# Kernel optimization log

Hardware: AMD Instinct MI355X
Metric: run time of the kernel (lower is better)

The kernel has to match this reference:

```python
import jax, jax.numpy as jnp
import numpy as np

B, W, CBLK, C, H, L, VOCAB = 8, 512, 24, 512, 8, 2, 256
HD = C // H


def _ln(x, g, b, eps=1e-5):
    m = x.mean(-1, keepdims=True)
    v = ((x - m) ** 2).mean(-1, keepdims=True)
    return (x - m) * jax.lax.rsqrt(v + eps) * g + b


def _causal_attn(q, k, v):
    # q,k,v: [..., T, hd]; causal softmax attention, scale 1/sqrt(hd)
    T = q.shape[-2]
    scale = 1.0 / (q.shape[-1] ** 0.5)
    s = jnp.einsum('...qd,...kd->...qk', q, k) * scale
    mask = jnp.tril(jnp.ones((T, T), dtype=bool))
    s = jnp.where(mask, s, jnp.finfo(s.dtype).min)
    return jnp.einsum('...qk,...kd->...qd', jax.nn.softmax(s, axis=-1), v)


def _mha_char(seq, w_qkv, last_ix):
    # seq: [B,W,c,C]; per-word causal char attention, then gather row last_ix
    b, w, c, _ = seq.shape
    q, k, v = jnp.split(seq @ w_qkv, 3, axis=-1)
    sh = lambda t: t.reshape(b, w, c, H, HD).transpose(0, 1, 3, 2, 4)
    o = _causal_attn(sh(q), sh(k), sh(v))          # [B,W,H,c,hd]
    o = o.transpose(0, 1, 3, 2, 4).reshape(b, w, c, C)
    return jnp.take_along_axis(o, last_ix[:, :, None, None], axis=2)[:, :, 0, :]


def _mha_word(x, w_qkv, w_proj):
    b, w, _ = x.shape
    q, k, v = jnp.split(x @ w_qkv, 3, axis=-1)
    sh = lambda t: t.reshape(b, w, H, HD).transpose(0, 2, 1, 3)
    o = _causal_attn(sh(q), sh(k), sh(v))
    o = o.transpose(0, 2, 1, 3).reshape(b, w, C)
    return o @ w_proj


def setup_inputs() -> dict:
    key = jax.random.key(0)
    ks = jax.random.split(key, 16)
    # ragged word lengths in [1, CBLK]; mask = ones then zeros (as produced by pad())
    lengths = jax.random.randint(ks[0], (B, W), 1, CBLK + 1)
    attention_mask = (jnp.arange(CBLK)[None, None, :] < lengths[:, :, None]).astype(jnp.int32)
    x = jax.random.randint(ks[1], (B, W, CBLK), 0, VOCAB).astype(jnp.int32)
    std = 0.02
    res_std = std * (2 * L) ** -0.5  # res_flag init scaling
    n = lambda k, s, sd=std: sd * jax.random.normal(k, s, dtype=jnp.float32)
    return dict(
        x=x, attention_mask=attention_mask,
        cte=n(ks[2], (VOCAB, C)), cpe=n(ks[3], (CBLK, C)), wpe=n(ks[4], (W, C)),
        ln1_g=jnp.ones((L, C)), ln1_b=jnp.zeros((L, C)),
        ln2_g=jnp.ones((L, C)), ln2_b=jnp.zeros((L, C)),
        ln3_g=jnp.ones((L, C)), ln3_b=jnp.zeros((L, C)),
        cattn_w=n(ks[5], (L, C, 3 * C)), cattn_proj=n(ks[6], (L, C, C)),
        wattn_w=n(ks[7], (L, C, 3 * C)), wattn_proj=n(ks[8], (L, C, C), res_std),
        mlp_fc=n(ks[9], (L, C, 4 * C)), mlp_proj=n(ks[10], (L, 4 * C, C), res_std),
        proj_w=n(ks[11], (C, CBLK * C)), lm_head_w=n(ks[12], (C, VOCAB)),
    )


def reference(x, attention_mask, cte, cpe, wpe, ln1_g, ln1_b, ln2_g, ln2_b, ln3_g, ln3_b,
              cattn_w, cattn_proj, wattn_w, wattn_proj, mlp_fc, mlp_proj, proj_w, lm_head_w):
    last_ix = attention_mask.sum(axis=2) - 1           # [B,W], last real char per word
    state = cte[x] + cpe[None, None, :, :]             # [B,W,c,C]
    context = None                                     # current_conv.context/pad, vectorized
    for l in range(L):
        if l == 0:
            # first_time: operate on full padded char sequences, cache ln_1 output
            hln = _ln(state, ln1_g[l], ln1_b[l])       # [B,W,c,C]
            context = hln
            seq = hln
        else:
            # splice the new word vector into position last_ix of the cached context
            hln = _ln(state, ln1_g[l], ln1_b[l])       # [B,W,C]
            repl = jnp.arange(CBLK)[None, None, :] == last_ix[:, :, None]
            seq = jnp.where(repl[..., None], hln[:, :, None, :], context)
        o = _mha_char(seq, cattn_w[l], last_ix)        # [B,W,C]
        if l == 0:
            o = o + wpe[None, :, :]                    # word pos emb added only first_time
        state = o @ cattn_proj[l]                      # note: no residual around c_attn
        state = state + _mha_word(_ln(state, ln2_g[l], ln2_b[l]), wattn_w[l], wattn_proj[l])
        hm = _ln(state, ln3_g[l], ln3_b[l])
        state = state + jax.nn.gelu(hm @ mlp_fc[l], approximate=False) @ mlp_proj[l]
    y = (state @ proj_w).reshape(B, W, CBLK, C)
    return y @ lm_head_w                               # logits [B,W,CBLK,VOCAB]
```

## Files before the change

kernel.cpp:

```cpp
#include <hip/hip_runtime.h>
#include <hip/hip_bf16.h>
#include <math.h>


namespace {

constexpr int Bn = 8, Wn = 512, CB = 24, Cd = 512, Hn = 8, Lln = 2, Vn = 256, HDn = 64;
constexpr int BW = Bn * Wn;
constexpr int C3 = 3 * Cd;
constexpr int FF = 4 * Cd;
constexpr int NROW = BW * CB;

typedef unsigned short u16;
typedef short short8 __attribute__((ext_vector_type(8)));
typedef float f32x4 __attribute__((ext_vector_type(4)));
typedef __attribute__((address_space(1))) void gvoid_t;
typedef __attribute__((address_space(3))) void lvoid_t;

__device__ __forceinline__ u16 f2bu(float f) {
  __hip_bfloat16 h = __float2bfloat16(f);
  return __builtin_bit_cast(u16, h);
}
__device__ __forceinline__ float bu2f(u16 u) {
  return __bfloat162float(__builtin_bit_cast(__hip_bfloat16, u));
}
__device__ __forceinline__ float geluf(float x) {
  return 0.5f * x * (1.0f + erff(x * 0.7071067811865475f));
}
__device__ __forceinline__ void gl16(const void* g, void* l) {
  __builtin_amdgcn_global_load_lds((gvoid_t*)g, (lvoid_t*)l, 16, 0, 0);
}

__global__ void k_lastix(const int* __restrict__ mask, int* __restrict__ lastix) {
  int i = blockIdx.x * 256 + threadIdx.x;
  if (i < BW) {
    int s = 0;
#pragma unroll
    for (int j = 0; j < CB; ++j) s += mask[i * CB + j];
    lastix[i] = s - 1;
  }
}

__device__ __forceinline__ void f2b8(const float* __restrict__ s, u16* __restrict__ d) {
  float4 a = *(const float4*)s;
  float4 b = *(const float4*)(s + 4);
  union { uint4 u; u16 h[8]; } pk;
  pk.h[0] = f2bu(a.x); pk.h[1] = f2bu(a.y); pk.h[2] = f2bu(a.z); pk.h[3] = f2bu(a.w);
  pk.h[4] = f2bu(b.x); pk.h[5] = f2bu(b.y); pk.h[6] = f2bu(b.z); pk.h[7] = f2bu(b.w);
  *(uint4*)d = pk.u;
}

__device__ __forceinline__ void wT_tile(const float* __restrict__ src, u16* __restrict__ dst,
                                        int K, int N, int n0, int k0,
                                        u16 T[64][72], int tid) {
  int kl = tid >> 2, nc = (tid & 3) * 16;
  const float* s = src + (long)(k0 + kl) * N + n0 + nc;
#pragma unroll
  for (int u = 0; u < 4; ++u) {
    float4 f = *(const float4*)(s + u * 4);
    T[nc + u * 4 + 0][kl] = f2bu(f.x);
    T[nc + u * 4 + 1][kl] = f2bu(f.y);
    T[nc + u * 4 + 2][kl] = f2bu(f.z);
    T[nc + u * 4 + 3][kl] = f2bu(f.w);
  }
  __syncthreads();
  int nl = tid >> 2, kc = (tid & 3) * 16;
  u16* d = dst + (long)(n0 + nl) * K + k0 + kc;
  *(uint4*)d = *(uint4*)&T[nl][kc];
  *(uint4*)(d + 8) = *(uint4*)&T[nl][kc + 8];
}

__global__ __launch_bounds__(256) void k_prep(
    const float* __restrict__ proj_w, u16* __restrict__ projwb,
    const float* __restrict__ cattn_w, u16* __restrict__ wcb,
    const float* __restrict__ lm_head, u16* __restrict__ lmhT,
    const float* __restrict__ cattn_proj, const float* __restrict__ wattn_w,
    const float* __restrict__ wattn_proj, const float* __restrict__ mlp_fc,
    const float* __restrict__ mlp_proj, u16* __restrict__ wT) {
  __shared__ u16 T[64][72];
  int b = blockIdx.x, tid = threadIdx.x;
  if (b < 3072) { long i = ((long)b * 256 + tid) * 8; f2b8(proj_w + i, projwb + i); return; }
  b -= 3072;
  if (b < 768) { long i = ((long)b * 256 + tid) * 8; f2b8(cattn_w + i, wcb + i); return; }
  b -= 768;
  if (b < 32) { wT_tile(lm_head, lmhT, Cd, Vn, (b & 3) * 64, (b >> 2) * 64, T, tid); return; }
  b -= 32;
  int l = b >> 10, r = b & 1023;
  size_t lw = (size_t)(2 * C3 * Cd + 2 * Cd * Cd + 2 * FF * Cd);
  u16* bl = wT + l * lw;
  const float* src; u16* dst; int K, N, nt;
  if (r < 192)      { src = cattn_w + (size_t)l * Cd * C3;    dst = bl;                              K = Cd; N = C3; nt = 24; }
  else if (r < 256) { src = cattn_proj + (size_t)l * Cd * Cd; dst = bl + C3 * Cd;                    K = Cd; N = Cd; nt = 8;  r -= 192; }
  else if (r < 448) { src = wattn_w + (size_t)l * Cd * C3;    dst = bl + C3 * Cd + Cd * Cd;          K = Cd; N = C3; nt = 24; r -= 256; }
  else if (r < 512) { src = wattn_proj + (size_t)l * Cd * Cd; dst = bl + 2 * C3 * Cd + Cd * Cd;      K = Cd; N = Cd; nt = 8;  r -= 448; }
  else if (r < 768) { src = mlp_fc + (size_t)l * Cd * FF;     dst = bl + 2 * C3 * Cd + 2 * Cd * Cd;  K = Cd; N = FF; nt = 32; r -= 512; }
  else              { src = mlp_proj + (size_t)l * FF * Cd;   dst = bl + 2 * C3 * Cd + 2 * Cd * Cd + FF * Cd; K = FF; N = Cd; nt = 8; r -= 768; }
  wT_tile(src, dst, K, N, (r % nt) * 64, (r / nt) * 64, T, tid);
}

__global__ __launch_bounds__(64) void k_embed_ln(
    const int* __restrict__ x, const float* __restrict__ cte, const float* __restrict__ cpe,
    const float* __restrict__ g, const float* __restrict__ b,
    const int* __restrict__ lastix, u16* __restrict__ ctx) {
  int r = blockIdx.x;
  int bw = r / CB, ch = r - bw * CB;
  if (ch > lastix[bw]) return;
  int tok = x[r];
  const float* e = cte + (long)tok * Cd;
  const float* pe = cpe + (long)ch * Cd;
  int lane = threadIdx.x;
  float v[8];
  float s = 0.f, sq = 0.f;
#pragma unroll
  for (int u = 0; u < 2; ++u) {
    float4 a = *(const float4*)(e + u * 256 + lane * 4);
    float4 p4 = *(const float4*)(pe + u * 256 + lane * 4);
    v[u * 4 + 0] = a.x + p4.x; v[u * 4 + 1] = a.y + p4.y;
    v[u * 4 + 2] = a.z + p4.z; v[u * 4 + 3] = a.w + p4.w;
  }
#pragma unroll
  for (int u = 0; u < 8; ++u) { s += v[u]; sq += v[u] * v[u]; }
#pragma unroll
  for (int m = 32; m; m >>= 1) { s += __shfl_xor(s, m); sq += __shfl_xor(sq, m); }
  float mean = s * (1.0f / Cd);
  float var = sq * (1.0f / Cd) - mean * mean;
  float rs = rsqrtf(var + 1e-5f);
  u16* o = ctx + (long)r * Cd;
#pragma unroll
  for (int u = 0; u < 2; ++u) {
    int c0 = u * 256 + lane * 4;
    float4 g4 = *(const float4*)(g + c0);
    float4 b4 = *(const float4*)(b + c0);
    float o0 = (v[u * 4 + 0] - mean) * rs * g4.x + b4.x;
    float o1 = (v[u * 4 + 1] - mean) * rs * g4.y + b4.y;
    float o2 = (v[u * 4 + 2] - mean) * rs * g4.z + b4.z;
    float o3 = (v[u * 4 + 3] - mean) * rs * g4.w + b4.w;
    uint2 w;
    w.x = (unsigned)f2bu(o0) | ((unsigned)f2bu(o1) << 16);
    w.y = (unsigned)f2bu(o2) | ((unsigned)f2bu(o3) << 16);
    *(uint2*)(o + c0) = w;
  }
}

__global__ __launch_bounds__(64) void k_ln(
    const float* __restrict__ X, u16* __restrict__ Y,
    const float* __restrict__ g, const float* __restrict__ b) {
  long r = blockIdx.x;
  const float* xr = X + r * Cd;
  int lane = threadIdx.x;
  float v[8];
  float s = 0.f, sq = 0.f;
#pragma unroll
  for (int u = 0; u < 2; ++u) {
    float4 a = *(const float4*)(xr + u * 256 + lane * 4);
    v[u * 4 + 0] = a.x; v[u * 4 + 1] = a.y; v[u * 4 + 2] = a.z; v[u * 4 + 3] = a.w;
  }
#pragma unroll
  for (int u = 0; u < 8; ++u) { s += v[u]; sq += v[u] * v[u]; }
#pragma unroll
  for (int m = 32; m; m >>= 1) { s += __shfl_xor(s, m); sq += __shfl_xor(sq, m); }
  float mean = s * (1.0f / Cd);
  float var = sq * (1.0f / Cd) - mean * mean;
  float rs = rsqrtf(var + 1e-5f);
  u16* o = Y + r * Cd;
#pragma unroll
  for (int u = 0; u < 2; ++u) {
    int c0 = u * 256 + lane * 4;
    float4 g4 = *(const float4*)(g + c0);
    float4 b4 = *(const float4*)(b + c0);
    float o0 = (v[u * 4 + 0] - mean) * rs * g4.x + b4.x;
    float o1 = (v[u * 4 + 1] - mean) * rs * g4.y + b4.y;
    float o2 = (v[u * 4 + 2] - mean) * rs * g4.z + b4.z;
    float o3 = (v[u * 4 + 3] - mean) * rs * g4.w + b4.w;
    uint2 w;
    w.x = (unsigned)f2bu(o0) | ((unsigned)f2bu(o1) << 16);
    w.y = (unsigned)f2bu(o2) | ((unsigned)f2bu(o3) << 16);
    *(uint2*)(o + c0) = w;
  }
}

__global__ __launch_bounds__(64) void k_gather_last(
    const u16* __restrict__ ctx, const int* __restrict__ lastix, u16* __restrict__ qin) {
  long bw = blockIdx.x;
  int r = (int)bw * CB + lastix[bw];
  const uint4* s = (const uint4*)(ctx + (long)r * Cd);
  uint4* d = (uint4*)(qin + bw * Cd);
  d[threadIdx.x] = s[threadIdx.x];
}

template <int BM, int BN, int EPI, int OUTBF>
__global__ __launch_bounds__(256) void k_mgemm(
    const u16* __restrict__ A, int lda, long sA1, long sA2,
    const u16* __restrict__ Bt, int ldb, long sB1, long sB2,
    void* __restrict__ Cv, int ldc, long sC1, long sC2,
    const float* __restrict__ R, u16* __restrict__ D2,
    const float* __restrict__ PL, const u16* __restrict__ VL,
    const float* __restrict__ WP, int K, int zdiv) {
  constexpr int WM = BM / 2;
  constexpr int WN = BN / 2;
  constexpr int FM = WM / 16, FN = WN / 16;
  __shared__ u16 As[BM * 32];
  __shared__ u16 Bs[BN * 32];
  long m0 = (long)blockIdx.y * BM, n0 = (long)blockIdx.x * BN;
  int z = blockIdx.z;
  int z1 = z / zdiv, z2 = z - z1 * zdiv;
  A += z1 * sA1 + z2 * sA2;
  Bt += z1 * sB1 + z2 * sB2;
  long coff = z1 * sC1 + z2 * sC2;
  int tid = threadIdx.x;
  int wid = tid >> 6, lane = tid & 63;
  int wr = wid >> 1, wc = wid & 1;

  const int srow = tid >> 2, skk = (tid & 3) * 8;
  const u16* Ald[BM / 64];
  const u16* Bld[BN / 64];
#pragma unroll
  for (int i = 0; i < BM / 64; ++i) Ald[i] = A + (m0 + srow + i * 64) * (long)lda + skk;
#pragma unroll
  for (int i = 0; i < BN / 64; ++i) Bld[i] = Bt + (n0 + srow + i * 64) * (long)ldb + skk;

  f32x4 acc[FM][FN] = {};
  const int fr = lane & 15, kg = lane >> 4;

  for (int k0 = 0; k0 < K; k0 += 32) {
#pragma unroll
    for (int i = 0; i < BM / 64; ++i) gl16(Ald[i] + k0, &As[(tid + i * 256) * 8]);
#pragma unroll
    for (int i = 0; i < BN / 64; ++i) gl16(Bld[i] + k0, &Bs[(tid + i * 256) * 8]);
    __syncthreads();
    short8 af[FM], bf[FN];
#pragma unroll
    for (int m = 0; m < FM; ++m)
      af[m] = *(const short8*)&As[(wr * WM + m * 16 + fr) * 32 + kg * 8];
#pragma unroll
    for (int n = 0; n < FN; ++n)
      bf[n] = *(const short8*)&Bs[(wc * WN + n * 16 + fr) * 32 + kg * 8];
#pragma unroll
    for (int m = 0; m < FM; ++m)
#pragma unroll
      for (int n = 0; n < FN; ++n)
        acc[m][n] = __builtin_amdgcn_mfma_f32_16x16x32_bf16(af[m], bf[n], acc[m][n], 0, 0, 0);
    __syncthreads();
  }
  int ccol = lane & 15, crow4 = (lane >> 4) * 4;
#pragma unroll
  for (int m = 0; m < FM; ++m)
#pragma unroll
    for (int n = 0; n < FN; ++n)
#pragma unroll
      for (int q = 0; q < 4; ++q) {
        long gr = m0 + wr * WM + m * 16 + crow4 + q;
        long gc = n0 + wc * WN + n * 16 + ccol;
        float v = acc[m][n][q];
        long idx = gr * (long)ldc + gc + coff;
        if (EPI == 1 || EPI == 3) v += R[idx];
        if (EPI == 2) v = geluf(v);
        if (EPI == 4) {
          v += PL[gr * 8 + z2] * bu2f(VL[gr * (long)C3 + 2 * Cd + z2 * 64 + gc]);
          if (WP) v += WP[(long)(gr & (Wn - 1)) * Cd + z2 * 64 + gc];
        }
        if (EPI == 3) {
          ((float*)Cv)[idx] = v;
          D2[idx] = f2bu(v);
        } else if (OUTBF) {
          ((u16*)Cv)[idx] = f2bu(v);
        } else {
          ((float*)Cv)[idx] = v;
        }
      }
}

__global__ __launch_bounds__(256) void k_cattn2(
    const u16* __restrict__ ctx, const u16* __restrict__ qtil,
    const u16* __restrict__ qkvc, const int* __restrict__ lastix,
    u16* __restrict__ U, float* __restrict__ plast) {
  constexpr int CS = 520;
  int gw = blockIdx.x;
  int li = lastix[gw];
  __shared__ u16 ctxs[CB - 1][CS];
  __shared__ float spf[4][Hn][32];
  __shared__ float sp[Hn][CB];
  int tid = threadIdx.x;
  for (int u = tid; u < li * 64; u += 256) {
    int row = u >> 6, c = (u & 63) * 8;
    *(uint4*)&ctxs[row][c] = *(const uint4*)(ctx + ((long)(gw * CB + row)) * Cd + c);
  }
  __syncthreads();
  int w = tid >> 6, lane = tid & 63;
  int fr = lane & 15, kg = lane >> 4;
  {
    const u16* qbase = qtil + (long)gw * 4096 + (fr & 7) * 512 + w * 128 + kg * 8;
    int r0 = fr;
    int r1 = 16 + fr; if (r1 > CB - 2) r1 = CB - 2;
    f32x4 acc0 = {}, acc1 = {};
#pragma unroll
    for (int kk = 0; kk < 4; ++kk) {
      short8 af = *(const short8*)(qbase + kk * 32);
      short8 b0 = *(const short8*)&ctxs[r0][w * 128 + kk * 32 + kg * 8];
      short8 b1 = *(const short8*)&ctxs[r1][w * 128 + kk * 32 + kg * 8];
      acc0 = __builtin_amdgcn_mfma_f32_16x16x32_bf16(af, b0, acc0, 0, 0, 0);
      acc1 = __builtin_amdgcn_mfma_f32_16x16x32_bf16(af, b1, acc1, 0, 0, 0);
    }
    if (lane < 32) {
      int jj = lane & 15;
#pragma unroll
      for (int q = 0; q < 4; ++q) {
        int h = (lane >> 4) * 4 + q;
        spf[w][h][jj] = acc0[q];
        spf[w][h][16 + jj] = acc1[q];
      }
    }
  }
  __syncthreads();
  {
    int h = tid >> 5, j = tid & 31;
    if (j < CB)
      sp[h][j] = (spf[0][h][j] + spf[1][h][j] + spf[2][h][j] + spf[3][h][j]) * 0.125f;
  }
  __syncthreads();
  if (tid < 8) {
    const u16* qq = qkvc + (long)gw * C3 + tid * 64;
    const u16* kk = qq + Cd;
    float s = 0.f;
#pragma unroll
    for (int u = 0; u < 64; ++u) s += bu2f(qq[u]) * bu2f(kk[u]);
    sp[tid][li] = s * 0.125f;
  }
  __syncthreads();
  if (tid < 8) {
    float m = -3.4e38f;
    for (int jj = 0; jj <= li; ++jj) m = fmaxf(m, sp[tid][jj]);
    float s = 0.f;
    for (int jj = 0; jj <= li; ++jj) { float e = expf(sp[tid][jj] - m); sp[tid][jj] = e; s += e; }
    float inv = 1.0f / s;
    for (int jj = 0; jj <= li; ++jj) sp[tid][jj] *= inv;
    plast[gw * 8 + tid] = sp[tid][li];
  }
  __syncthreads();
  int h = tid >> 5, d0 = (tid & 31) * 16;
  float uacc[16];
#pragma unroll
  for (int i = 0; i < 16; ++i) uacc[i] = 0.f;
  for (int jj = 0; jj < li; ++jj) {
    float p = sp[h][jj];
    const u16* cv = &ctxs[jj][d0];
#pragma unroll
    for (int i = 0; i < 16; ++i) uacc[i] += p * bu2f(cv[i]);
  }
  union { uint4 q[2]; u16 hh[16]; } pk;
#pragma unroll
  for (int i = 0; i < 16; ++i) pk.hh[i] = f2bu(uacc[i]);
  u16* d = U + (long)gw * 4096 + h * 512 + d0;
  *(uint4*)d = pk.q[0];
  *(uint4*)(d + 8) = pk.q[1];
}

__global__ __launch_bounds__(256) void k_vt(const u16* __restrict__ qkv, u16* __restrict__ Vt) {
  __shared__ u16 T[64][72];
  int z = blockIdx.y, jt = blockIdx.x;
  int b = z >> 3, h = z & 7;
  int tid = threadIdx.x;
  int jl = tid >> 2, dc = (tid & 3) * 16;
  const u16* s = qkv + ((long)(b * Wn + jt * 64 + jl)) * C3 + 2 * Cd + h * HDn + dc;
  *(uint4*)&T[jl][dc] = *(const uint4*)s;
  *(uint4*)&T[jl][dc + 8] = *(const uint4*)(s + 8);
  __syncthreads();
  int dl = tid >> 2, jc = (tid & 3) * 16;
  u16 tmp[16];
#pragma unroll
  for (int u = 0; u < 16; ++u) tmp[u] = T[jc + u][dl];
  u16* d = Vt + (long)z * HDn * Wn + (long)dl * Wn + jt * 64 + jc;
  *(uint4*)d = *(uint4*)&tmp[0];
  *(uint4*)(d + 8) = *(uint4*)&tmp[8];
}

__global__ __launch_bounds__(256) void k_fattn(
    const u16* __restrict__ qkv, const u16* __restrict__ Vt, u16* __restrict__ ao) {
  constexpr int ST = 68;
  __shared__ u16 Ks[64 * ST];
  __shared__ u16 Vs[64 * ST];
  __shared__ u16 Ps[4][16 * ST];
  int qt = blockIdx.x;
  int z  = blockIdx.y;
  int b = z >> 3, h = z & 7;
  int tid = threadIdx.x;
  int w = tid >> 6, lane = tid & 63;
  int fr = lane & 15, kg = lane >> 4;

  short8 qf[2];
  {
    const u16* qp = qkv + ((long)(b * Wn + qt * 64 + w * 16 + fr)) * C3 + h * 64 + kg * 8;
    qf[0] = *(const short8*)qp;
    qf[1] = *(const short8*)(qp + 32);
  }
  f32x4 oacc[4] = {};
  float mrow[4], lrow[4];
#pragma unroll
  for (int q = 0; q < 4; ++q) { mrow[q] = -3.4e38f; lrow[q] = 0.f; }

  for (int kt = 0; kt <= qt; ++kt) {
    __syncthreads();
    {
      int r = tid >> 2, c = (tid & 3) * 16;
      const u16* kp = qkv + ((long)(b * Wn + kt * 64 + r)) * C3 + Cd + h * 64 + c;
      *(uint4*)&Ks[r * ST + c] = *(const uint4*)kp;
      *(uint4*)&Ks[r * ST + c + 8] = *(const uint4*)(kp + 8);
      const u16* vp = Vt + (long)z * (64 * Wn) + (long)r * Wn + kt * 64 + c;
      *(uint4*)&Vs[r * ST + c] = *(const uint4*)vp;
      *(uint4*)&Vs[r * ST + c + 8] = *(const uint4*)(vp + 8);
    }
    __syncthreads();
    f32x4 s[4];
#pragma unroll
    for (int n = 0; n < 4; ++n) {
      short8 kf0 = *(const short8*)&Ks[(n * 16 + fr) * ST + kg * 8];
      short8 kf1 = *(const short8*)&Ks[(n * 16 + fr) * ST + kg * 8 + 32];
      f32x4 a = {};
      a = __builtin_amdgcn_mfma_f32_16x16x32_bf16(qf[0], kf0, a, 0, 0, 0);
      a = __builtin_amdgcn_mfma_f32_16x16x32_bf16(qf[1], kf1, a, 0, 0, 0);
      s[n] = a;
    }
    int irow0 = qt * 64 + w * 16 + kg * 4;
#pragma unroll
    for (int n = 0; n < 4; ++n) {
      int jcol = kt * 64 + n * 16 + fr;
#pragma unroll
      for (int q = 0; q < 4; ++q) {
        float v = s[n][q] * 0.125f;
        s[n][q] = (jcol > irow0 + q) ? -3.4e38f : v;
      }
    }
    float sf[4];
#pragma unroll
    for (int q = 0; q < 4; ++q) {
      float mm = fmaxf(fmaxf(s[0][q], s[1][q]), fmaxf(s[2][q], s[3][q]));
      mm = fmaxf(mm, __shfl_xor(mm, 1));
      mm = fmaxf(mm, __shfl_xor(mm, 2));
      mm = fmaxf(mm, __shfl_xor(mm, 4));
      mm = fmaxf(mm, __shfl_xor(mm, 8));
      float mnew = fmaxf(mrow[q], mm);
      sf[q] = expf(mrow[q] - mnew);
      mrow[q] = mnew;
    }
    float ls[4] = {0.f, 0.f, 0.f, 0.f};
#pragma unroll
    for (int n = 0; n < 4; ++n) {
#pragma unroll
      for (int q = 0; q < 4; ++q) {
        float p = expf(s[n][q] - mrow[q]);
        u16 pb = f2bu(p);
        ls[q] += bu2f(pb);
        Ps[w][(kg * 4 + q) * ST + n * 16 + fr] = pb;
      }
    }
#pragma unroll
    for (int q = 0; q < 4; ++q) {
      float l = ls[q];
      l += __shfl_xor(l, 1); l += __shfl_xor(l, 2);
      l += __shfl_xor(l, 4); l += __shfl_xor(l, 8);
      lrow[q] = lrow[q] * sf[q] + l;
#pragma unroll
      for (int n = 0; n < 4; ++n) oacc[n][q] *= sf[q];
    }
    asm volatile("s_waitcnt lgkmcnt(0)" ::: "memory");
    short8 pa0 = *(const short8*)&Ps[w][fr * ST + kg * 8];
    short8 pa1 = *(const short8*)&Ps[w][fr * ST + kg * 8 + 32];
#pragma unroll
    for (int n = 0; n < 4; ++n) {
      short8 vf0 = *(const short8*)&Vs[(n * 16 + fr) * ST + kg * 8];
      short8 vf1 = *(const short8*)&Vs[(n * 16 + fr) * ST + kg * 8 + 32];
      oacc[n] = __builtin_amdgcn_mfma_f32_16x16x32_bf16(pa0, vf0, oacc[n], 0, 0, 0);
      oacc[n] = __builtin_amdgcn_mfma_f32_16x16x32_bf16(pa1, vf1, oacc[n], 0, 0, 0);
    }
  }
  int orow = b * Wn + qt * 64 + w * 16 + kg * 4;
#pragma unroll
  for (int q = 0; q < 4; ++q) {
    float inv = 1.0f / lrow[q];
#pragma unroll
    for (int n = 0; n < 4; ++n)
      ao[(long)(orow + q) * Cd + h * 64 + n * 16 + fr] = f2bu(oacc[n][q] * inv);
  }
}

template <int BM, int BN, int EPI, int OUTBF>
static inline void mgemm(hipStream_t st,
    const u16* A, int lda, long sA1, long sA2,
    const u16* Bt, int ldb, long sB1, long sB2,
    void* C, int ldc, long sC1, long sC2,
    const float* R, int M, int N, int K, int nz, int zdiv,
    u16* D2 = nullptr, const float* PL = nullptr, const u16* VL = nullptr,
    const float* WP = nullptr) {
  dim3 g(N / BN, (M + BM - 1) / BM, nz);
  hipLaunchKernelGGL((k_mgemm<BM, BN, EPI, OUTBF>), g, dim3(256), 0, st,
                     A, lda, sA1, sA2, Bt, ldb, sB1, sB2, C, ldc, sC1, sC2,
                     R ? R : (const float*)C, D2, PL, VL, WP, K, zdiv);
}

}

extern "C" void kernel_launch(void* const* d_in, const int* in_sizes, int n_in,
                              void* d_out, int out_size, void* d_ws, size_t ws_size,
                              hipStream_t stream) {
  (void)in_sizes; (void)n_in; (void)out_size; (void)ws_size;
  const int*   x          = (const int*)d_in[0];
  const int*   amask      = (const int*)d_in[1];
  const float* cte        = (const float*)d_in[2];
  const float* cpe        = (const float*)d_in[3];
  const float* wpe        = (const float*)d_in[4];
  const float* ln1g       = (const float*)d_in[5];
  const float* ln1b       = (const float*)d_in[6];
  const float* ln2g       = (const float*)d_in[7];
  const float* ln2b       = (const float*)d_in[8];
  const float* ln3g       = (const float*)d_in[9];
  const float* ln3b       = (const float*)d_in[10];
  const float* cattn_w    = (const float*)d_in[11];
  const float* cattn_proj = (const float*)d_in[12];
  const float* wattn_w    = (const float*)d_in[13];
  const float* wattn_proj = (const float*)d_in[14];
  const float* mlp_fc     = (const float*)d_in[15];
  const float* mlp_proj   = (const float*)d_in[16];
  const float* proj_w     = (const float*)d_in[17];
  const float* lm_head    = (const float*)d_in[18];
  float* out = (float*)d_out;

  char* base = (char*)d_ws;
  size_t off = 0;
  auto alloc = [&](size_t bytes) -> char* {
    char* r = base + off;
    off += (bytes + 255) & ~(size_t)255;
    return r;
  };
  int*   lastix = (int*)alloc((size_t)BW * 4);
  float* plast  = (float*)alloc((size_t)BW * 8 * 4);
  u16*   ctx    = (u16*)alloc((size_t)NROW * Cd * 2);
  char*  big    = alloc((size_t)105 * 1024 * 1024);
  u16*   kvq    = (u16*)alloc((size_t)BW * C3 * 2);
  u16*   qin    = (u16*)alloc((size_t)BW * Cd * 2);
  float* state  = (float*)alloc((size_t)BW * Cd * 4);
  u16*   stateb = (u16*)alloc((size_t)BW * Cd * 2);
  u16*   hln    = (u16*)alloc((size_t)BW * Cd * 2);
  u16*   ao     = (u16*)alloc((size_t)BW * Cd * 2);
  u16*   wT     = (u16*)alloc((size_t)2 * (2 * C3 * Cd + 2 * Cd * Cd + 2 * FF * Cd) * 2);
  u16*   wcb    = (u16*)alloc((size_t)2 * Cd * C3 * 2);
  u16*   projwb = (u16*)alloc((size_t)Cd * CB * Cd * 2);
  u16*   lmhT   = (u16*)alloc((size_t)Vn * Cd * 2);

  u16*   U     = (u16*)big;
  u16*   qtil  = (u16*)(big + (size_t)35651584);
  u16*   Vt    = (u16*)(big + (size_t)71303168);
  u16*   mlph  = (u16*)big;
  u16*   combT = (u16*)big;

  size_t lw = (size_t)(2 * C3 * Cd + 2 * Cd * Cd + 2 * FF * Cd);
  auto cwT    = [&](int l) { return wT + l * lw; };
  auto cprojT = [&](int l) { return wT + l * lw + C3 * Cd; };
  auto wwT    = [&](int l) { return wT + l * lw + C3 * Cd + Cd * Cd; };
  auto wprojT = [&](int l) { return wT + l * lw + 2 * C3 * Cd + Cd * Cd; };
  auto fcT    = [&](int l) { return wT + l * lw + 2 * C3 * Cd + 2 * Cd * Cd; };
  auto mprojT = [&](int l) { return wT + l * lw + 2 * C3 * Cd + 2 * Cd * Cd + FF * Cd; };

  hipLaunchKernelGGL(k_lastix, dim3(16), dim3(256), 0, stream, amask, lastix);
  hipLaunchKernelGGL(k_prep, dim3(5920), dim3(256), 0, stream,
                     proj_w, projwb, cattn_w, wcb, lm_head, lmhT,
                     cattn_proj, wattn_w, wattn_proj, mlp_fc, mlp_proj, wT);
  hipLaunchKernelGGL(k_embed_ln, dim3(NROW), dim3(64), 0, stream,
                     x, cte, cpe, ln1g, ln1b, lastix, ctx);

  for (int l = 0; l < Lln; ++l) {
    u16* qkvc = kvq;
    u16* qkvw = kvq;
    if (l == 0)
      hipLaunchKernelGGL(k_gather_last, dim3(BW), dim3(64), 0, stream, ctx, lastix, qin);
    else
      hipLaunchKernelGGL(k_ln, dim3(BW), dim3(64), 0, stream, state, qin, ln1g + Cd, ln1b + Cd);
    mgemm<128, 64, 0, 1>(stream, qin, Cd, 0, 0, cwT(l), Cd, 0, 0,
                         qkvc, C3, 0, 0, nullptr, BW, C3, Cd, 1, 1);
    mgemm<64, 64, 0, 1>(stream, qkvc, C3, 0, 64,
                        wcb + (size_t)l * Cd * C3 + Cd, C3, 0, 64,
                        qtil, 8 * Cd, 0, Cd, nullptr, BW, Cd, HDn, 8, 8);
    hipLaunchKernelGGL(k_cattn2, dim3(BW), dim3(256), 0, stream,
                       ctx, qtil, qkvc, lastix, U, plast);
    mgemm<64, 64, 4, 1>(stream, U, 8 * Cd, 0, Cd,
                        cwT(l) + (size_t)(2 * Cd) * Cd, Cd, 0, (long)HDn * Cd,
                        ao, Cd, 0, HDn, nullptr, BW, HDn, Cd, 8, 8,
                        nullptr, plast, qkvc, l == 0 ? wpe : nullptr);
    mgemm<64, 64, 0, 0>(stream, ao, Cd, 0, 0, cprojT(l), Cd, 0, 0,
                        state, Cd, 0, 0, nullptr, BW, Cd, Cd, 1, 1);
    hipLaunchKernelGGL(k_ln, dim3(BW), dim3(64), 0, stream, state, hln, ln2g + l * Cd, ln2b + l * Cd);
    mgemm<128, 64, 0, 1>(stream, hln, Cd, 0, 0, wwT(l), Cd, 0, 0,
                         qkvw, C3, 0, 0, nullptr, BW, C3, Cd, 1, 1);
    hipLaunchKernelGGL(k_vt, dim3(Wn / 64, 64), dim3(256), 0, stream, qkvw, Vt);
    hipLaunchKernelGGL(k_fattn, dim3(8, 64), dim3(256), 0, stream, qkvw, Vt, ao);
    mgemm<64, 64, 1, 0>(stream, ao, Cd, 0, 0, wprojT(l), Cd, 0, 0,
                        state, Cd, 0, 0, state, BW, Cd, Cd, 1, 1);
    hipLaunchKernelGGL(k_ln, dim3(BW), dim3(64), 0, stream, state, hln, ln3g + l * Cd, ln3b + l * Cd);
    mgemm<64, 64, 2, 1>(stream, hln, Cd, 0, 0, fcT(l), Cd, 0, 0,
                        mlph, FF, 0, 0, nullptr, BW, FF, Cd, 1, 1);
    mgemm<64, 64, 3, 0>(stream, mlph, FF, 0, 0, mprojT(l), FF, 0, 0,
                        state, Cd, 0, 0, state, BW, Cd, FF, 1, 1, stateb);
  }

  mgemm<64, 64, 0, 1>(stream, lmhT, Cd, 0, 0,
                      projwb, CB * Cd, 0, Cd,
                      combT, Cd, 0, (long)Vn * Cd,
                      nullptr, Vn, Cd, Cd, CB, CB);
  mgemm<128, 128, 0, 0>(stream, stateb, Cd, 0, 0, combT, Cd, 0, 0,
                        out, CB * Vn, 0, 0, nullptr, BW, CB * Vn, Cd, 1, 1);
}
```

Before: 543.6 us.

## Double-buffer K/V tiles in word attention and pack four rows per row-kernel block

The flash attention kernel now prefetches the next K and V tiles into registers while it computes on the current tile, then writes them into a second shared-memory buffer. This drops one barrier per iteration and hides global load latency. The LayerNorm, embed-LN and gather kernels now process four rows per 256-thread block instead of one row per 64-thread block, cutting the block count. The prefetch doubles the K/V shared memory and adds registers, which may lower occupancy.

```diff
diff --git a/kernel.cpp b/kernel.cpp
--- a/kernel.cpp
+++ b/kernel.cpp
@@ -98,17 +98,17 @@
   wT_tile(src, dst, K, N, (r % nt) * 64, (r / nt) * 64, T, tid);
 }
 
-__global__ __launch_bounds__(64) void k_embed_ln(
+__global__ __launch_bounds__(256) void k_embed_ln(
     const int* __restrict__ x, const float* __restrict__ cte, const float* __restrict__ cpe,
     const float* __restrict__ g, const float* __restrict__ b,
     const int* __restrict__ lastix, u16* __restrict__ ctx) {
-  int r = blockIdx.x;
+  int r = blockIdx.x * 4 + (threadIdx.x >> 6);
   int bw = r / CB, ch = r - bw * CB;
   if (ch > lastix[bw]) return;
   int tok = x[r];
   const float* e = cte + (long)tok * Cd;
   const float* pe = cpe + (long)ch * Cd;
-  int lane = threadIdx.x;
+  int lane = threadIdx.x & 63;
   float v[8];
   float s = 0.f, sq = 0.f;
 #pragma unroll
@@ -142,12 +142,12 @@
   }
 }
 
-__global__ __launch_bounds__(64) void k_ln(
+__global__ __launch_bounds__(256) void k_ln(
     const float* __restrict__ X, u16* __restrict__ Y,
     const float* __restrict__ g, const float* __restrict__ b) {
-  long r = blockIdx.x;
+  long r = blockIdx.x * 4 + (threadIdx.x >> 6);
   const float* xr = X + r * Cd;
-  int lane = threadIdx.x;
+  int lane = threadIdx.x & 63;
   float v[8];
   float s = 0.f, sq = 0.f;
 #pragma unroll
@@ -179,13 +179,12 @@
   }
 }
 
-__global__ __launch_bounds__(64) void k_gather_last(
+__global__ __launch_bounds__(256) void k_gather_last(
     const u16* __restrict__ ctx, const int* __restrict__ lastix, u16* __restrict__ qin) {
-  long bw = blockIdx.x;
+  long bw = blockIdx.x * 4 + (threadIdx.x >> 6);
+  int lane = threadIdx.x & 63;
   int r = (int)bw * CB + lastix[bw];
-  const uint4* s = (const uint4*)(ctx + (long)r * Cd);
-  uint4* d = (uint4*)(qin + bw * Cd);
-  d[threadIdx.x] = s[threadIdx.x];
+  ((uint4*)(qin + bw * Cd))[lane] = ((const uint4*)(ctx + (long)r * Cd))[lane];
 }
 
 template <int BM, int BN, int EPI, int OUTBF>
@@ -377,8 +376,8 @@
 __global__ __launch_bounds__(256) void k_fattn(
     const u16* __restrict__ qkv, const u16* __restrict__ Vt, u16* __restrict__ ao) {
   constexpr int ST = 68;
-  __shared__ u16 Ks[64 * ST];
-  __shared__ u16 Vs[64 * ST];
+  __shared__ u16 Ks[2][64 * ST];
+  __shared__ u16 Vs[2][64 * ST];
   __shared__ u16 Ps[4][16 * ST];
   int qt = blockIdx.x;
   int z  = blockIdx.y;
@@ -393,6 +392,23 @@
     qf[0] = *(const short8*)qp;
     qf[1] = *(const short8*)(qp + 32);
   }
+  int sr = tid >> 2, sc = (tid & 3) * 16;
+  const u16* kbase = qkv + ((long)(b * Wn + sr)) * C3 + Cd + h * 64 + sc;
+  const u16* vbase = Vt + (long)z * (64 * Wn) + (long)sr * Wn + sc;
+  uint4 kr0, kr1, vr0, vr1;
+  auto LD = [&](int kt) {
+    const u16* kp = kbase + (long)kt * 64 * C3;
+    kr0 = *(const uint4*)kp; kr1 = *(const uint4*)(kp + 8);
+    const u16* vp = vbase + kt * 64;
+    vr0 = *(const uint4*)vp; vr1 = *(const uint4*)(vp + 8);
+  };
+  auto WR = [&](int buf) {
+    *(uint4*)&Ks[buf][sr * ST + sc] = kr0; *(uint4*)&Ks[buf][sr * ST + sc + 8] = kr1;
+    *(uint4*)&Vs[buf][sr * ST + sc] = vr0; *(uint4*)&Vs[buf][sr * ST + sc + 8] = vr1;
+  };
+  LD(0); WR(0);
+  int cur = 0;
+
   f32x4 oacc[4] = {};
   float mrow[4], lrow[4];
 #pragma unroll
@@ -400,21 +416,14 @@
 
   for (int kt = 0; kt <= qt; ++kt) {
     __syncthreads();
-    {
-      int r = tid >> 2, c = (tid & 3) * 16;
-      const u16* kp = qkv + ((long)(b * Wn + kt * 64 + r)) * C3 + Cd + h * 64 + c;
-      *(uint4*)&Ks[r * ST + c] = *(const uint4*)kp;
-      *(uint4*)&Ks[r * ST + c + 8] = *(const uint4*)(kp + 8);
-      const u16* vp = Vt + (long)z * (64 * Wn) + (long)r * Wn + kt * 64 + c;
-      *(uint4*)&Vs[r * ST + c] = *(const uint4*)vp;
-      *(uint4*)&Vs[r * ST + c + 8] = *(const uint4*)(vp + 8);
-    }
-    __syncthreads();
+    if (kt < qt) LD(kt + 1);
+    const u16* Kc = Ks[cur];
+    const u16* Vc = Vs[cur];
     f32x4 s[4];
 #pragma unroll
     for (int n = 0; n < 4; ++n) {
-      short8 kf0 = *(const short8*)&Ks[(n * 16 + fr) * ST + kg * 8];
-      short8 kf1 = *(const short8*)&Ks[(n * 16 + fr) * ST + kg * 8 + 32];
+      short8 kf0 = *(const short8*)&Kc[(n * 16 + fr) * ST + kg * 8];
+      short8 kf1 = *(const short8*)&Kc[(n * 16 + fr) * ST + kg * 8 + 32];
       f32x4 a = {};
       a = __builtin_amdgcn_mfma_f32_16x16x32_bf16(qf[0], kf0, a, 0, 0, 0);
       a = __builtin_amdgcn_mfma_f32_16x16x32_bf16(qf[1], kf1, a, 0, 0, 0);
@@ -467,11 +476,13 @@
     short8 pa1 = *(const short8*)&Ps[w][fr * ST + kg * 8 + 32];
 #pragma unroll
     for (int n = 0; n < 4; ++n) {
-      short8 vf0 = *(const short8*)&Vs[(n * 16 + fr) * ST + kg * 8];
-      short8 vf1 = *(const short8*)&Vs[(n * 16 + fr) * ST + kg * 8 + 32];
+      short8 vf0 = *(const short8*)&Vc[(n * 16 + fr) * ST + kg * 8];
+      short8 vf1 = *(const short8*)&Vc[(n * 16 + fr) * ST + kg * 8 + 32];
       oacc[n] = __builtin_amdgcn_mfma_f32_16x16x32_bf16(pa0, vf0, oacc[n], 0, 0, 0);
       oacc[n] = __builtin_amdgcn_mfma_f32_16x16x32_bf16(pa1, vf1, oacc[n], 0, 0, 0);
     }
+    if (kt < qt) WR(cur ^ 1);
+    cur ^= 1;
   }
   int orow = b * Wn + qt * 64 + w * 16 + kg * 4;
 #pragma unroll
@@ -564,16 +575,16 @@
   hipLaunchKernelGGL(k_prep, dim3(5920), dim3(256), 0, stream,
                      proj_w, projwb, cattn_w, wcb, lm_head, lmhT,
                      cattn_proj, wattn_w, wattn_proj, mlp_fc, mlp_proj, wT);
-  hipLaunchKernelGGL(k_embed_ln, dim3(NROW), dim3(64), 0, stream,
+  hipLaunchKernelGGL(k_embed_ln, dim3(NROW / 4), dim3(256), 0, stream,
                      x, cte, cpe, ln1g, ln1b, lastix, ctx);
 
   for (int l = 0; l < Lln; ++l) {
     u16* qkvc = kvq;
     u16* qkvw = kvq;
     if (l == 0)
-      hipLaunchKernelGGL(k_gather_last, dim3(BW), dim3(64), 0, stream, ctx, lastix, qin);
+      hipLaunchKernelGGL(k_gather_last, dim3(BW / 4), dim3(256), 0, stream, ctx, lastix, qin);
     else
-      hipLaunchKernelGGL(k_ln, dim3(BW), dim3(64), 0, stream, state, qin, ln1g + Cd, ln1b + Cd);
+      hipLaunchKernelGGL(k_ln, dim3(BW / 4), dim3(256), 0, stream, state, qin, ln1g + Cd, ln1b + Cd);
     mgemm<128, 64, 0, 1>(stream, qin, Cd, 0, 0, cwT(l), Cd, 0, 0,
                          qkvc, C3, 0, 0, nullptr, BW, C3, Cd, 1, 1);
     mgemm<64, 64, 0, 1>(stream, qkvc, C3, 0, 64,
@@ -587,14 +598,14 @@
                         nullptr, plast, qkvc, l == 0 ? wpe : nullptr);
     mgemm<64, 64, 0, 0>(stream, ao, Cd, 0, 0, cprojT(l), Cd, 0, 0,
                         state, Cd, 0, 0, nullptr, BW, Cd, Cd, 1, 1);
-    hipLaunchKernelGGL(k_ln, dim3(BW), dim3(64), 0, stream, state, hln, ln2g + l * Cd, ln2b + l * Cd);
+    hipLaunchKernelGGL(k_ln, dim3(BW / 4), dim3(256), 0, stream, state, hln, ln2g + l * Cd, ln2b + l * Cd);
     mgemm<128, 64, 0, 1>(stream, hln, Cd, 0, 0, wwT(l), Cd, 0, 0,
                          qkvw, C3, 0, 0, nullptr, BW, C3, Cd, 1, 1);
     hipLaunchKernelGGL(k_vt, dim3(Wn / 64, 64), dim3(256), 0, stream, qkvw, Vt);
     hipLaunchKernelGGL(k_fattn, dim3(8, 64), dim3(256), 0, stream, qkvw, Vt, ao);
     mgemm<64, 64, 1, 0>(stream, ao, Cd, 0, 0, wprojT(l), Cd, 0, 0,
                         state, Cd, 0, 0, state, BW, Cd, Cd, 1, 1);
-    hipLaunchKernelGGL(k_ln, dim3(BW), dim3(64), 0, stream, state, hln, ln3g + l * Cd, ln3b + l * Cd);
+    hipLaunchKernelGGL(k_ln, dim3(BW / 4), dim3(256), 0, stream, state, hln, ln3g + l * Cd, ln3b + l * Cd);
     mgemm<64, 64, 2, 1>(stream, hln, Cd, 0, 0, fcT(l), Cd, 0, 0,
                         mlph, FF, 0, 0, nullptr, BW, FF, Cd, 1, 1);
     mgemm<64, 64, 3, 0>(stream, mlph, FF, 0, 0, mprojT(l), FF, 0, 0,
```

Measured after the change: 572.2 us. 5.3% more time.
